# Optimization experiments

Measured on AMD Instinct MI355X. Metric: run time of the kernel, lower is better.

The kernel has to match this reference:

```python
import jax, jax.numpy as jnp
import numpy as np

EPS = 1e-8  # torch F.cosine_similarity default eps
MARGIN = 1.0


def _pair_indices(p_lens, n_lens):
    """Build gather indices for the ragged all-pairs (positive x negative) expansion.
    For batch i, pair order is lexicographic (j, k): positive j repeated n_i times,
    negative segment tiled p_i times -- exactly matching the torch repeat/repeat_interleave.
    Host-side numpy (lens are concrete integers)."""
    p = np.asarray(p_lens, dtype=np.int64)
    n = np.asarray(n_lens, dtype=np.int64)
    pairs = p * n                                   # per-example pair counts
    total = int(pairs.sum())
    p_off = np.concatenate([[0], np.cumsum(p)[:-1]])
    n_off = np.concatenate([[0], np.cumsum(n)[:-1]])
    pair_off = np.concatenate([[0], np.cumsum(pairs)[:-1]])
    a_idx = np.repeat(np.arange(len(p)), pairs)     # [total]
    t = np.arange(total) - np.repeat(pair_off, pairs)   # local pair position in [0, p_i*n_i)
    n_rep = np.repeat(n, pairs)
    j = t // n_rep                                  # positive index within segment
    k = t % n_rep                                   # negative index within segment
    p_idx = np.repeat(p_off, pairs) + j
    n_idx = np.repeat(n_off, pairs) + k
    return jnp.asarray(a_idx), jnp.asarray(p_idx), jnp.asarray(n_idx)


def _cosine(x, y):
    dot = jnp.sum(x * y, axis=-1)
    nx = jnp.linalg.norm(x, axis=-1)
    ny = jnp.linalg.norm(y, axis=-1)
    return dot / jnp.maximum(nx * ny, EPS)


def setup_inputs() -> dict:
    rng = np.random.default_rng(0)
    bs, dim = 1024, 768
    p_lens = rng.integers(1, 13, size=bs)
    n_lens = rng.integers(1, 13, size=bs)
    key = jax.random.key(0)
    k1, k2, k3 = jax.random.split(key, 3)
    anchor = jax.random.normal(k1, (bs, dim), dtype=jnp.float32)
    positive = jax.random.normal(k2, (int(p_lens.sum()), dim), dtype=jnp.float32)
    negative = jax.random.normal(k3, (int(n_lens.sum()), dim), dtype=jnp.float32)
    return {
        "anchor": anchor,
        "positive": positive,
        "negative": negative,
        "positive_lens": jnp.asarray(p_lens, dtype=jnp.int32),
        "negative_lens": jnp.asarray(n_lens, dtype=jnp.int32),
    }


def reference(anchor, positive, negative, positive_lens, negative_lens):
    a_idx, p_idx, n_idx = _pair_indices(positive_lens, negative_lens)
    a = anchor[a_idx]       # [total_pairs, dim]
    pp = positive[p_idx]
    nn_ = negative[n_idx]
    d_ap = 1.0 - _cosine(a, pp)
    d_an = 1.0 - _cosine(a, nn_)
    # TripletMarginWithDistanceLoss, swap=False, reduction='mean'
    loss = jnp.mean(jnp.maximum(d_ap - d_an + MARGIN, 0.0))
    return loss
```

## Files before the change

### kernel.cpp

```cpp
#include <hip/hip_runtime.h>
#include <hip/hip_bf16.h>

#define DIM 768
#define EPS 1e-8f

__global__ __launch_bounds__(1024) void scan_kernel(
    const int* __restrict__ p_lens, const int* __restrict__ n_lens,
    int* __restrict__ p_off, int* __restrict__ n_off,
    int* __restrict__ total, float* __restrict__ out, int bs)
{
    __shared__ int sp[1024];
    __shared__ int sn[1024];
    __shared__ int st[1024];
    int tid = threadIdx.x;
    int p = (tid < bs) ? p_lens[tid] : 0;
    int n = (tid < bs) ? n_lens[tid] : 0;
    sp[tid] = p;
    sn[tid] = n;
    st[tid] = p * n;
    __syncthreads();
    for (int off = 1; off < 1024; off <<= 1) {
        int vp = (tid >= off) ? sp[tid - off] : 0;
        int vn = (tid >= off) ? sn[tid - off] : 0;
        __syncthreads();
        sp[tid] += vp;
        sn[tid] += vn;
        __syncthreads();
    }
    if (tid < bs) {
        p_off[tid] = sp[tid] - p;
        n_off[tid] = sn[tid] - n;
    }
    for (int s = 512; s > 0; s >>= 1) {
        if (tid < s) st[tid] += st[tid + s];
        __syncthreads();
    }
    if (tid == 0) {
        *total = st[0];
        *out = 0.0f;
    }
}

__global__ __launch_bounds__(256) void triplet_kernel(
    const float* __restrict__ anchor, const float* __restrict__ positive,
    const float* __restrict__ negative,
    const int* __restrict__ p_lens, const int* __restrict__ n_lens,
    const int* __restrict__ p_off_arr, const int* __restrict__ n_off_arr,
    const int* __restrict__ total_ptr, float* __restrict__ out)
{
    const int b = blockIdx.x;
    const int tid = threadIdx.x;
    const int wave = tid >> 6;
    const int lane = tid & 63;

    __shared__ float sA[DIM];
    __shared__ float sCos[32];
    __shared__ float sRed[4];
    __shared__ float sAnorm;

    const int pl = p_lens[b];
    const int nl = n_lens[b];
    const int po = p_off_arr[b];
    const int no = n_off_arr[b];

    const float4* a4 = (const float4*)(anchor + (size_t)b * DIM);
    float asq = 0.0f;
    for (int q = tid; q < DIM / 4; q += 256) {
        float4 v = a4[q];
        ((float4*)sA)[q] = v;
        asq += v.x * v.x + v.y * v.y + v.z * v.z + v.w * v.w;
    }
    #pragma unroll
    for (int s = 32; s > 0; s >>= 1) asq += __shfl_xor(asq, s);
    if (lane == 0) sRed[wave] = asq;
    __syncthreads();
    if (tid == 0) sAnorm = sqrtf(sRed[0] + sRed[1] + sRed[2] + sRed[3]);
    __syncthreads();
    const float an = sAnorm;

    const int nvec = pl + nl;
    for (int v = wave; v < nvec; v += 4) {
        const float* x = (v < pl)
            ? positive + (size_t)(po + v) * DIM
            : negative + (size_t)(no + (v - pl)) * DIM;
        const float4* x4 = (const float4*)x;
        float dot = 0.0f, nx = 0.0f;
        #pragma unroll
        for (int q = 0; q < 3; ++q) {
            float4 xv = x4[lane + 64 * q];
            float4 av = ((const float4*)sA)[lane + 64 * q];
            dot += av.x * xv.x + av.y * xv.y + av.z * xv.z + av.w * xv.w;
            nx  += xv.x * xv.x + xv.y * xv.y + xv.z * xv.z + xv.w * xv.w;
        }
        #pragma unroll
        for (int s = 32; s > 0; s >>= 1) {
            dot += __shfl_xor(dot, s);
            nx  += __shfl_xor(nx, s);
        }
        if (lane == 0) sCos[v] = dot / fmaxf(an * sqrtf(nx), EPS);
    }
    __syncthreads();

    const int pairs = pl * nl;
    float s = 0.0f;
    for (int t = tid; t < pairs; t += 256) {
        int j = t / nl;
        int k = t - j * nl;
        s += fmaxf(sCos[pl + k] - sCos[j] + 1.0f, 0.0f);
    }
    #pragma unroll
    for (int sh = 32; sh > 0; sh >>= 1) s += __shfl_xor(s, sh);
    if (lane == 0) sRed[wave] = s;
    __syncthreads();
    if (tid == 0) {
        float blk = sRed[0] + sRed[1] + sRed[2] + sRed[3];
        atomicAdd(out, blk / (float)(*total_ptr));
    }
}

extern "C" void kernel_launch(void* const* d_in, const int* in_sizes, int n_in,
                              void* d_out, int out_size, void* d_ws, size_t ws_size,
                              hipStream_t stream) {
    const float* anchor   = (const float*)d_in[0];
    const float* positive = (const float*)d_in[1];
    const float* negative = (const float*)d_in[2];
    const int*   p_lens   = (const int*)d_in[3];
    const int*   n_lens   = (const int*)d_in[4];
    float* out = (float*)d_out;

    const int bs = in_sizes[3];

    int* p_off = (int*)d_ws;
    int* n_off = p_off + bs;
    int* total = n_off + bs;

    scan_kernel<<<1, 1024, 0, stream>>>(p_lens, n_lens, p_off, n_off, total, out, bs);
    triplet_kernel<<<bs, 256, 0, stream>>>(anchor, positive, negative,
                                           p_lens, n_lens, p_off, n_off, total, out);
}
```

Measured before the change: 101.8 us.

## Fuse offset scan into triplet kernel with per-block redundant prefix sums

Removes the separate single-block scan kernel. Each block now computes its own positive and negative offsets and the total pair count by reducing over the length arrays, and the output is zeroed with a memset. This drops one serialized kernel launch and its global round trip. In exchange every block re-reads the 1024-entry length arrays, which adds redundant work and L2 traffic per block.

Result: no change. 100.3 us (-1.5%).

```diff
diff --git a/kernel.cpp b/kernel.cpp
--- a/kernel.cpp
+++ b/kernel.cpp
@@ -4,49 +4,11 @@
 #define DIM 768
 #define EPS 1e-8f
 
-__global__ __launch_bounds__(1024) void scan_kernel(
-    const int* __restrict__ p_lens, const int* __restrict__ n_lens,
-    int* __restrict__ p_off, int* __restrict__ n_off,
-    int* __restrict__ total, float* __restrict__ out, int bs)
-{
-    __shared__ int sp[1024];
-    __shared__ int sn[1024];
-    __shared__ int st[1024];
-    int tid = threadIdx.x;
-    int p = (tid < bs) ? p_lens[tid] : 0;
-    int n = (tid < bs) ? n_lens[tid] : 0;
-    sp[tid] = p;
-    sn[tid] = n;
-    st[tid] = p * n;
-    __syncthreads();
-    for (int off = 1; off < 1024; off <<= 1) {
-        int vp = (tid >= off) ? sp[tid - off] : 0;
-        int vn = (tid >= off) ? sn[tid - off] : 0;
-        __syncthreads();
-        sp[tid] += vp;
-        sn[tid] += vn;
-        __syncthreads();
-    }
-    if (tid < bs) {
-        p_off[tid] = sp[tid] - p;
-        n_off[tid] = sn[tid] - n;
-    }
-    for (int s = 512; s > 0; s >>= 1) {
-        if (tid < s) st[tid] += st[tid + s];
-        __syncthreads();
-    }
-    if (tid == 0) {
-        *total = st[0];
-        *out = 0.0f;
-    }
-}
-
-__global__ __launch_bounds__(256) void triplet_kernel(
+__global__ __launch_bounds__(256) void triplet_fused(
     const float* __restrict__ anchor, const float* __restrict__ positive,
     const float* __restrict__ negative,
     const int* __restrict__ p_lens, const int* __restrict__ n_lens,
-    const int* __restrict__ p_off_arr, const int* __restrict__ n_off_arr,
-    const int* __restrict__ total_ptr, float* __restrict__ out)
+    float* __restrict__ out, int bs)
 {
     const int b = blockIdx.x;
     const int tid = threadIdx.x;
@@ -55,13 +17,10 @@
 
     __shared__ float sA[DIM];
     __shared__ float sCos[32];
-    __shared__ float sRed[4];
+    __shared__ float sRedF[4];
+    __shared__ int   sRedI[4][3];
     __shared__ float sAnorm;
-
-    const int pl = p_lens[b];
-    const int nl = n_lens[b];
-    const int po = p_off_arr[b];
-    const int no = n_off_arr[b];
+    __shared__ int   sPO, sNO, sTot;
 
     const float4* a4 = (const float4*)(anchor + (size_t)b * DIM);
     float asq = 0.0f;
@@ -70,13 +29,40 @@
         ((float4*)sA)[q] = v;
         asq += v.x * v.x + v.y * v.y + v.z * v.z + v.w * v.w;
     }
+
+    int pre_p = 0, pre_n = 0, tot = 0;
+    for (int i = tid; i < bs; i += 256) {
+        int p = p_lens[i];
+        int n = n_lens[i];
+        if (i < b) { pre_p += p; pre_n += n; }
+        tot += p * n;
+    }
+
     #pragma unroll
-    for (int s = 32; s > 0; s >>= 1) asq += __shfl_xor(asq, s);
-    if (lane == 0) sRed[wave] = asq;
+    for (int s = 32; s > 0; s >>= 1) {
+        asq   += __shfl_xor(asq, s);
+        pre_p += __shfl_xor(pre_p, s);
+        pre_n += __shfl_xor(pre_n, s);
+        tot   += __shfl_xor(tot, s);
+    }
+    if (lane == 0) {
+        sRedF[wave] = asq;
+        sRedI[wave][0] = pre_p;
+        sRedI[wave][1] = pre_n;
+        sRedI[wave][2] = tot;
+    }
     __syncthreads();
-    if (tid == 0) sAnorm = sqrtf(sRed[0] + sRed[1] + sRed[2] + sRed[3]);
+    if (tid == 0) {
+        sAnorm = sqrtf(sRedF[0] + sRedF[1] + sRedF[2] + sRedF[3]);
+        sPO  = sRedI[0][0] + sRedI[1][0] + sRedI[2][0] + sRedI[3][0];
+        sNO  = sRedI[0][1] + sRedI[1][1] + sRedI[2][1] + sRedI[3][1];
+        sTot = sRedI[0][2] + sRedI[1][2] + sRedI[2][2] + sRedI[3][2];
+    }
+    const int pl = p_lens[b];
+    const int nl = n_lens[b];
     __syncthreads();
     const float an = sAnorm;
+    const int po = sPO, no = sNO;
 
     const int nvec = pl + nl;
     for (int v = wave; v < nvec; v += 4) {
@@ -110,11 +96,11 @@
     }
     #pragma unroll
     for (int sh = 32; sh > 0; sh >>= 1) s += __shfl_xor(s, sh);
-    if (lane == 0) sRed[wave] = s;
+    if (lane == 0) sRedF[wave] = s;
     __syncthreads();
     if (tid == 0) {
-        float blk = sRed[0] + sRed[1] + sRed[2] + sRed[3];
-        atomicAdd(out, blk / (float)(*total_ptr));
+        float blk = sRedF[0] + sRedF[1] + sRedF[2] + sRedF[3];
+        atomicAdd(out, blk / (float)sTot);
     }
 }
 
@@ -130,11 +116,7 @@
 
     const int bs = in_sizes[3];
 
-    int* p_off = (int*)d_ws;
-    int* n_off = p_off + bs;
-    int* total = n_off + bs;
-
-    scan_kernel<<<1, 1024, 0, stream>>>(p_lens, n_lens, p_off, n_off, total, out, bs);
-    triplet_kernel<<<bs, 256, 0, stream>>>(anchor, positive, negative,
-                                           p_lens, n_lens, p_off, n_off, total, out);
+    hipMemsetAsync(out, 0, sizeof(float), stream);
+    triplet_fused<<<bs, 256, 0, stream>>>(anchor, positive, negative,
+                                          p_lens, n_lens, out, bs);
 }
```
